# Kernel tuning notes

Hardware: AMD Instinct MI355X
Metric: run time of the kernel (lower is better)

The kernel has to match this reference:

```python
import jax, jax.numpy as jnp
import numpy as np

N_NODES = 10000
N_EDGES = 160000
IN_DIM = 512
HID = 256
HEADS = 4
OUT_DIM = 512
NEG_SLOPE = 0.2  # PyG GATConv default


def _glorot(key, shape):
    fan_in, fan_out = shape[0], shape[-1]
    lim = jnp.sqrt(6.0 / (fan_in + fan_out))
    return jax.random.uniform(key, shape, jnp.float32, -lim, lim)


def setup_inputs() -> dict:
    key = jax.random.key(0)
    ks = jax.random.split(key, 16)
    x = jax.random.normal(ks[0], (N_NODES, IN_DIM), jnp.float32)
    edge_index = jax.random.randint(ks[1], (2, N_EDGES), 0, N_NODES, jnp.int64)
    # layer 1: GATConv(512 -> 256, heads=4, concat) -> out 1024
    W1 = _glorot(ks[2], (IN_DIM, HEADS * HID))
    att_src1 = _glorot(ks[3], (HEADS, HID))
    att_dst1 = _glorot(ks[4], (HEADS, HID))
    b1 = jnp.zeros((HEADS * HID,), jnp.float32)
    # layer 2: GATConv(1024 -> 256, heads=4, concat) -> out 1024
    W2 = _glorot(ks[5], (HEADS * HID, HEADS * HID))
    att_src2 = _glorot(ks[6], (HEADS, HID))
    att_dst2 = _glorot(ks[7], (HEADS, HID))
    b2 = jnp.zeros((HEADS * HID,), jnp.float32)
    # final fc: 1024 -> 512
    fcW = _glorot(ks[8], (HEADS * HID, OUT_DIM))
    fcb = jnp.zeros((OUT_DIM,), jnp.float32)
    return dict(x=x, edge_index=edge_index, W1=W1, att_src1=att_src1,
                att_dst1=att_dst1, b1=b1, W2=W2, att_src2=att_src2,
                att_dst2=att_dst2, b2=b2, fcW=fcW, fcb=fcb)


def gat_conv(x, src, dst, W, att_src, att_dst, bias):
    # x: [N, F_in]; src/dst: [E] (self-loops already included)
    N = x.shape[0]
    h = (x @ W).reshape(N, HEADS, HID)                       # [N, H, C]
    a_src = jnp.sum(h * att_src, axis=-1)                    # [N, H]
    a_dst = jnp.sum(h * att_dst, axis=-1)                    # [N, H]
    e = jax.nn.leaky_relu(a_src[src] + a_dst[dst], NEG_SLOPE)  # [E, H]
    # numerically stable segment softmax over destination nodes
    m = jax.ops.segment_max(e, dst, num_segments=N)          # [N, H]
    e = jnp.exp(e - m[dst])
    s = jax.ops.segment_sum(e, dst, num_segments=N)          # [N, H]
    alpha = e / (s[dst] + 1e-16)                             # [E, H]
    msg = alpha[:, :, None] * h[src]                         # [E, H, C]
    out = jax.ops.segment_sum(msg, dst, num_segments=N)      # [N, H, C]
    return out.reshape(N, HEADS * HID) + bias


def reference(x, edge_index, W1, att_src1, att_dst1, b1,
              W2, att_src2, att_dst2, b2, fcW, fcb):
    N = x.shape[0]
    loops = jnp.arange(N, dtype=edge_index.dtype)
    src = jnp.concatenate([edge_index[0], loops])  # PyG add_self_loops=True
    dst = jnp.concatenate([edge_index[1], loops])
    h = gat_conv(x, src, dst, W1, att_src1, att_dst1, b1)
    h = jax.nn.relu(h)  # dropout is identity in eval mode
    h = gat_conv(h, src, dst, W2, att_src2, att_dst2, b2)
    h = jax.nn.relu(h)
    return h @ fcW + fcb
```

## Files before the change

kernel.cpp:

```cpp
#include <hip/hip_runtime.h>
#include <hip/hip_bf16.h>

#define NN 10000
#define NE 160000
#define NET 170000
#define IN_DIM 512
#define D1 1024
#define HEADS 4
#define HID 256
#define OUT_DIM 512
#define NEG_SLOPE 0.2f

typedef __attribute__((ext_vector_type(8))) short bf16x8;
typedef __attribute__((ext_vector_type(4))) float f32x4;

__device__ inline float b2f(unsigned short b) {
    union { unsigned u; float f; } x; x.u = ((unsigned)b) << 16; return x.f;
}
__device__ inline unsigned short f2b(float f) {
    union { float f; unsigned u; } x; x.f = f;
    unsigned u = x.u;
    unsigned r = u + 0x7FFFu + ((u >> 16) & 1u);
    return (unsigned short)(r >> 16);
}
__device__ inline float lrelu(float v) { return v > 0.f ? v : NEG_SLOPE * v; }

__global__ void init_kernel(const int* ei32, int* flag, int* counts, int* cursor) {
    int i = blockIdx.x * blockDim.x + threadIdx.x;
    if (i < NN) { counts[i] = 0; cursor[i] = 0; }
    if (blockIdx.x == 0) {
        __shared__ int nz;
        if (threadIdx.x == 0) nz = 0;
        __syncthreads();
        int acc = 0;
        for (int k = threadIdx.x; k < 500; k += 256) acc |= ei32[2 * k + 1];
        if (acc) atomicOr(&nz, 1);
        __syncthreads();
        if (threadIdx.x == 0) flag[0] = (nz == 0) ? 1 : 0;
    }
}

__device__ inline void load_edge(const void* ei, int f64, int e, int& s, int& d) {
    if (f64) {
        const long long* p = (const long long*)ei;
        s = (int)p[e]; d = (int)p[NE + e];
    } else {
        const int* p = (const int*)ei;
        s = p[e]; d = p[NE + e];
    }
}

__global__ void count_kernel(const void* ei, const int* flag, int* counts) {
    int e = blockIdx.x * blockDim.x + threadIdx.x;
    if (e >= NET) return;
    int s, d;
    if (e < NE) load_edge(ei, *flag, e, s, d);
    else d = e - NE;
    atomicAdd(&counts[d], 1);
}

__global__ __launch_bounds__(256) void scan_kernel(const int* counts, int* indptr) {
    __shared__ int part[256];
    int t = threadIdx.x;
    int base = t * 40;
    int local[40];
    int sum = 0;
#pragma unroll
    for (int k = 0; k < 40; k++) {
        int i = base + k;
        int c = (i < NN) ? counts[i] : 0;
        local[k] = sum;
        sum += c;
    }
    part[t] = sum;
    __syncthreads();
    for (int off = 1; off < 256; off <<= 1) {
        int v = (t >= off) ? part[t - off] : 0;
        __syncthreads();
        part[t] += v;
        __syncthreads();
    }
    int excl = part[t] - sum;
#pragma unroll
    for (int k = 0; k < 40; k++) {
        int i = base + k;
        if (i < NN) indptr[i] = excl + local[k];
    }
    if (t == 255) indptr[NN] = part[255];
}

__global__ void fill_kernel(const void* ei, const int* flag, const int* indptr,
                            int* cursor, int* csr_src) {
    int e = blockIdx.x * blockDim.x + threadIdx.x;
    if (e >= NET) return;
    int s, d;
    if (e < NE) load_edge(ei, *flag, e, s, d);
    else { s = e - NE; d = s; }
    int pos = indptr[d] + atomicAdd(&cursor[d], 1);
    csr_src[pos] = s;
}

__device__ void tpose_tile(const float* __restrict__ in, unsigned short* __restrict__ out,
                           int R, int C, int bx, int by) {
    __shared__ float tile[32][33];
    int tx = threadIdx.x & 31, ty = threadIdx.x >> 5;
    int c = bx * 32 + tx;
#pragma unroll
    for (int r0 = 0; r0 < 32; r0 += 8) {
        int r = by * 32 + ty + r0;
        tile[ty + r0][tx] = in[(size_t)r * C + c];
    }
    __syncthreads();
    int oc = by * 32 + tx;
#pragma unroll
    for (int r0 = 0; r0 < 32; r0 += 8) {
        int orow = bx * 32 + ty + r0;
        out[(size_t)orow * R + oc] = f2b(tile[tx][ty + r0]);
    }
}

#define CVT_NB 5000
#define TP1_NB 512
#define TP2_NB 1024
#define TP3_NB 512
__global__ __launch_bounds__(256) void prep_kernel(
    const float* __restrict__ x, unsigned short* __restrict__ xb,
    const float* __restrict__ W1, unsigned short* __restrict__ W1t,
    const float* __restrict__ W2, unsigned short* __restrict__ W2t,
    const float* __restrict__ fcW, unsigned short* __restrict__ fcWt) {
    int b = blockIdx.x;
    if (b < CVT_NB) {
        int i = b * 256 + threadIdx.x;
        float4 v = reinterpret_cast<const float4*>(x)[i];
        ushort4 o;
        o.x = f2b(v.x); o.y = f2b(v.y); o.z = f2b(v.z); o.w = f2b(v.w);
        reinterpret_cast<ushort4*>(xb)[i] = o;
        return;
    }
    b -= CVT_NB;
    if (b < TP1_NB) { tpose_tile(W1, W1t, IN_DIM, D1, b & 31, b >> 5); return; }
    b -= TP1_NB;
    if (b < TP2_NB) { tpose_tile(W2, W2t, D1, D1, b & 31, b >> 5); return; }
    b -= TP2_NB;
    tpose_tile(fcW, fcWt, D1, OUT_DIM, b & 15, b >> 4);
}

#define BM 128
#define BN 128
#define BK 64
__global__ __launch_bounds__(256) void gemm128(
    const unsigned short* __restrict__ A, const unsigned short* __restrict__ B,
    const float* __restrict__ bias, float* __restrict__ Cf, unsigned short* __restrict__ Cb,
    int M, int N, int K, int NB) {
    __shared__ __align__(16) unsigned short As[BM * BK];
    __shared__ __align__(16) unsigned short Bs[BN * BK];
    int t = threadIdx.x;
    int nwg = gridDim.x;
    int q = nwg >> 3, r = nwg & 7;
    int xcd = blockIdx.x & 7, jj = blockIdx.x >> 3;
    int wg = (xcd < r ? xcd * (q + 1) : r * (q + 1) + (xcd - r) * q) + jj;
    int row0 = (wg / NB) * BM, col0 = (wg % NB) * BN;

    int w = t >> 6, l = t & 63;
    int wr = w >> 1, wc = w & 1;
    f32x4 acc[4][4] = {};

    int srow = w * 8 + (l >> 3);
    int scs = (((l & 7) ^ (l >> 3)) * 8);
    const unsigned short* ap0 = A + (size_t)min(row0 +  0 + srow, M - 1) * K + scs;
    const unsigned short* ap1 = A + (size_t)min(row0 + 32 + srow, M - 1) * K + scs;
    const unsigned short* ap2 = A + (size_t)min(row0 + 64 + srow, M - 1) * K + scs;
    const unsigned short* ap3 = A + (size_t)min(row0 + 96 + srow, M - 1) * K + scs;
    const unsigned short* bp0 = B + (size_t)(col0 +  0 + srow) * K + scs;
    const unsigned short* bp1 = B + (size_t)(col0 + 32 + srow) * K + scs;
    const unsigned short* bp2 = B + (size_t)(col0 + 64 + srow) * K + scs;
    const unsigned short* bp3 = B + (size_t)(col0 + 96 + srow) * K + scs;
    unsigned short* asd0 = As + 0 * 2048 + w * 512;
    unsigned short* asd1 = As + 1 * 2048 + w * 512;
    unsigned short* asd2 = As + 2 * 2048 + w * 512;
    unsigned short* asd3 = As + 3 * 2048 + w * 512;
    unsigned short* bsd0 = Bs + 0 * 2048 + w * 512;
    unsigned short* bsd1 = Bs + 1 * 2048 + w * 512;
    unsigned short* bsd2 = Bs + 2 * 2048 + w * 512;
    unsigned short* bsd3 = Bs + 3 * 2048 + w * 512;

    int rr = l & 15;
    int rb = (rr & 7) << 4;
    int kb0 = (l >> 4) << 4;
    const char* Ab = (const char*)As;
    const char* Bb = (const char*)Bs;

#define GLD(src, dst) __builtin_amdgcn_global_load_lds( \
        (const __attribute__((address_space(1))) void*)(src), \
        (__attribute__((address_space(3))) void*)(dst), 16, 0, 0)

    for (int k0 = 0; k0 < K; k0 += BK) {
        GLD(ap0, asd0); GLD(ap1, asd1); GLD(ap2, asd2); GLD(ap3, asd3);
        GLD(bp0, bsd0); GLD(bp1, bsd1); GLD(bp2, bsd2); GLD(bp3, bsd3);
        ap0 += BK; ap1 += BK; ap2 += BK; ap3 += BK;
        bp0 += BK; bp1 += BK; bp2 += BK; bp3 += BK;
        __syncthreads();

#pragma unroll
        for (int ks = 0; ks < 2; ks++) {
            int kb = ((ks << 6) | kb0) ^ rb;
            bf16x8 af[4], bfv[4];
#pragma unroll
            for (int mi = 0; mi < 4; mi++)
                af[mi] = *reinterpret_cast<const bf16x8*>(
                    Ab + (wr * 64 + mi * 16 + rr) * 128 + kb);
#pragma unroll
            for (int ni = 0; ni < 4; ni++)
                bfv[ni] = *reinterpret_cast<const bf16x8*>(
                    Bb + (wc * 64 + ni * 16 + rr) * 128 + kb);
#pragma unroll
            for (int mi = 0; mi < 4; mi++)
#pragma unroll
                for (int ni = 0; ni < 4; ni++)
                    acc[mi][ni] = __builtin_amdgcn_mfma_f32_16x16x32_bf16(
                        af[mi], bfv[ni], acc[mi][ni], 0, 0, 0);
        }
        __syncthreads();
    }
#undef GLD

    int c_l = l & 15, r_h = (l >> 4) * 4;
#pragma unroll
    for (int mi = 0; mi < 4; mi++)
#pragma unroll
        for (int ni = 0; ni < 4; ni++) {
            int gc = col0 + wc * 64 + ni * 16 + c_l;
#pragma unroll
            for (int j = 0; j < 4; j++) {
                int gr = row0 + wr * 64 + mi * 16 + r_h + j;
                if (gr < M) {
                    float v = acc[mi][ni][j];
                    if (bias) v += bias[gc];
                    if (Cf) Cf[(size_t)gr * N + gc] = v;
                    if (Cb) Cb[(size_t)gr * N + gc] = f2b(v);
                }
            }
        }
}

__global__ __launch_bounds__(256) void att_kernel(const unsigned short* __restrict__ hb,
                                                  const float* __restrict__ att_s,
                                                  const float* __restrict__ att_d,
                                                  float* __restrict__ aS, float* __restrict__ aD) {
    int node = blockIdx.x * 4 + (threadIdx.x >> 6);
    int l = threadIdx.x & 63;
    int head = l >> 4, qq = l & 15;
    const unsigned short* hrow = hb + (size_t)node * D1 + head * HID + qq * 16;
    bf16x8 h0 = *reinterpret_cast<const bf16x8*>(hrow);
    bf16x8 h1 = *reinterpret_cast<const bf16x8*>(hrow + 8);
    const float* asp = att_s + head * HID + qq * 16;
    const float* adp = att_d + head * HID + qq * 16;
    float ps = 0.f, pd = 0.f;
#pragma unroll
    for (int c = 0; c < 8; c++) {
        float hv = b2f((unsigned short)h0[c]);
        float hw = b2f((unsigned short)h1[c]);
        ps += hv * asp[c] + hw * asp[8 + c];
        pd += hv * adp[c] + hw * adp[8 + c];
    }
#pragma unroll
    for (int off = 1; off <= 8; off <<= 1) {
        ps += __shfl_xor(ps, off);
        pd += __shfl_xor(pd, off);
    }
    if (qq == 0) {
        aS[node * HEADS + head] = ps;
        aD[node * HEADS + head] = pd;
    }
}

__global__ __launch_bounds__(256) void agg_kernel(const unsigned short* __restrict__ hb,
                                                  const float* __restrict__ aS,
                                                  const float* __restrict__ aD,
                                                  const int* __restrict__ indptr,
                                                  const int* __restrict__ csr_src,
                                                  const float* __restrict__ bias,
                                                  unsigned short* __restrict__ outb) {
    int node = blockIdx.x * 4 + (threadIdx.x >> 6);
    int l = threadIdx.x & 63;
    int head = l >> 4;
    int beg = indptr[node];
    int deg = indptr[node + 1] - beg;
    float adst = aD[node * HEADS + head];
    const unsigned short* hp = hb + (size_t)l * 16;
    const int* cs = csr_src + beg;
    float acc[16];
#pragma unroll
    for (int c = 0; c < 16; c++) acc[c] = 0.f;
    float esum = 0.f;
    int dm = deg - 1;
    for (int j = 0; j < deg; j += 4) {
        int i0 = j, i1 = min(j + 1, dm), i2 = min(j + 2, dm), i3 = min(j + 3, dm);
        int s0 = cs[i0], s1 = cs[i1], s2 = cs[i2], s3 = cs[i3];
        const unsigned short* r0 = hp + (size_t)s0 * D1;
        const unsigned short* r1 = hp + (size_t)s1 * D1;
        const unsigned short* r2 = hp + (size_t)s2 * D1;
        const unsigned short* r3 = hp + (size_t)s3 * D1;
        bf16x8 r0a = *reinterpret_cast<const bf16x8*>(r0);
        bf16x8 r0b = *reinterpret_cast<const bf16x8*>(r0 + 8);
        bf16x8 r1a = *reinterpret_cast<const bf16x8*>(r1);
        bf16x8 r1b = *reinterpret_cast<const bf16x8*>(r1 + 8);
        bf16x8 r2a = *reinterpret_cast<const bf16x8*>(r2);
        bf16x8 r2b = *reinterpret_cast<const bf16x8*>(r2 + 8);
        bf16x8 r3a = *reinterpret_cast<const bf16x8*>(r3);
        bf16x8 r3b = *reinterpret_cast<const bf16x8*>(r3 + 8);
        float e0 = __expf(lrelu(aS[s0 * HEADS + head] + adst));
        float e1 = (j + 1 <= dm) ? __expf(lrelu(aS[s1 * HEADS + head] + adst)) : 0.f;
        float e2 = (j + 2 <= dm) ? __expf(lrelu(aS[s2 * HEADS + head] + adst)) : 0.f;
        float e3 = (j + 3 <= dm) ? __expf(lrelu(aS[s3 * HEADS + head] + adst)) : 0.f;
        esum += e0 + e1 + e2 + e3;
#pragma unroll
        for (int c = 0; c < 8; c++) {
            acc[c] += e0 * b2f((unsigned short)r0a[c]) + e1 * b2f((unsigned short)r1a[c])
                    + e2 * b2f((unsigned short)r2a[c]) + e3 * b2f((unsigned short)r3a[c]);
            acc[8 + c] += e0 * b2f((unsigned short)r0b[c]) + e1 * b2f((unsigned short)r1b[c])
                        + e2 * b2f((unsigned short)r2b[c]) + e3 * b2f((unsigned short)r3b[c]);
        }
    }
    float inv = 1.f / (esum + 1e-16f);
    const float* bp = bias + l * 16;
    bf16x8 o0, o1;
#pragma unroll
    for (int c = 0; c < 8; c++) {
        o0[c] = (short)f2b(fmaxf(acc[c] * inv + bp[c], 0.f));
        o1[c] = (short)f2b(fmaxf(acc[8 + c] * inv + bp[8 + c], 0.f));
    }
    unsigned short* op = outb + (size_t)node * D1 + l * 16;
    *reinterpret_cast<bf16x8*>(op) = o0;
    *reinterpret_cast<bf16x8*>(op + 8) = o1;
}

extern "C" void kernel_launch(void* const* d_in, const int* in_sizes, int n_in,
                              void* d_out, int out_size, void* d_ws, size_t ws_size,
                              hipStream_t stream) {
    const float* x   = (const float*)d_in[0];
    const void*  ei  = d_in[1];
    const float* W1  = (const float*)d_in[2];
    const float* as1 = (const float*)d_in[3];
    const float* ad1 = (const float*)d_in[4];
    const float* b1  = (const float*)d_in[5];
    const float* W2  = (const float*)d_in[6];
    const float* as2 = (const float*)d_in[7];
    const float* ad2 = (const float*)d_in[8];
    const float* b2  = (const float*)d_in[9];
    const float* fcW = (const float*)d_in[10];
    const float* fcb = (const float*)d_in[11];
    float* out = (float*)d_out;

    char* ws = (char*)d_ws;
    size_t o = 0;
    auto carve = [&](size_t bytes) -> char* {
        char* p = ws + o;
        o = (o + bytes + 255) & ~(size_t)255;
        return p;
    };
    unsigned short* xb   = (unsigned short*)carve((size_t)NN * IN_DIM * 2);
    unsigned short* hb   = (unsigned short*)carve((size_t)NN * D1 * 2);
    unsigned short* x2b  = (unsigned short*)carve((size_t)NN * D1 * 2);
    unsigned short* W1t  = (unsigned short*)carve((size_t)D1 * IN_DIM * 2);
    unsigned short* W2t  = (unsigned short*)carve((size_t)D1 * D1 * 2);
    unsigned short* fcWt = (unsigned short*)carve((size_t)OUT_DIM * D1 * 2);
    float* aS   = (float*)carve((size_t)NN * HEADS * 4);
    float* aD   = (float*)carve((size_t)NN * HEADS * 4);
    int* counts = (int*)carve((size_t)NN * 4);
    int* cursor = (int*)carve((size_t)NN * 4);
    int* indptr = (int*)carve((size_t)(NN + 1) * 4);
    int* csr_src= (int*)carve((size_t)NET * 4);
    int* flag   = (int*)carve(4);
    (void)ws_size; (void)in_sizes; (void)n_in; (void)out_size;

    init_kernel<<<(NN + 255) / 256, 256, 0, stream>>>((const int*)ei, flag, counts, cursor);
    count_kernel<<<(NET + 255) / 256, 256, 0, stream>>>(ei, flag, counts);
    scan_kernel<<<1, 256, 0, stream>>>(counts, indptr);
    fill_kernel<<<(NET + 255) / 256, 256, 0, stream>>>(ei, flag, indptr, cursor, csr_src);

    prep_kernel<<<CVT_NB + TP1_NB + TP2_NB + TP3_NB, 256, 0, stream>>>(
        x, xb, W1, W1t, W2, W2t, fcW, fcWt);

    const int MB = (NN + BM - 1) / BM;
    gemm128<<<MB * (D1 / BN), 256, 0, stream>>>(xb, W1t, nullptr, nullptr, hb,
                                                NN, D1, IN_DIM, D1 / BN);
    att_kernel<<<NN / 4, 256, 0, stream>>>(hb, as1, ad1, aS, aD);
    agg_kernel<<<NN / 4, 256, 0, stream>>>(hb, aS, aD, indptr, csr_src, b1, x2b);
    gemm128<<<MB * (D1 / BN), 256, 0, stream>>>(x2b, W2t, nullptr, nullptr, hb,
                                                NN, D1, D1, D1 / BN);
    att_kernel<<<NN / 4, 256, 0, stream>>>(hb, as2, ad2, aS, aD);
    agg_kernel<<<NN / 4, 256, 0, stream>>>(hb, aS, aD, indptr, csr_src, b2, x2b);
    gemm128<<<MB * (OUT_DIM / BN), 256, 0, stream>>>(x2b, fcWt, fcb, out, nullptr,
                                                     NN, OUT_DIM, D1, OUT_DIM / BN);
}
```

Baseline: 269.2 us.

## Split aggregation across eight column-slice blocks per node group with 2-channel lanes

The aggregation kernel now launches eight blocks per group of four nodes, each covering a 128-column slice (half a head). Each lane handles two bf16 channels instead of sixteen, and the edge loop is unrolled to eight neighbours. The aim is more parallelism, lower register pressure and better occupancy, with coalesced 256-byte row segments per wave. In exchange, index loads and exp computations are repeated eight times per node, and each lane's gather loads are narrow 4-byte accesses.

```diff
diff --git a/kernel.cpp b/kernel.cpp
--- a/kernel.cpp
+++ b/kernel.cpp
@@ -281,58 +281,55 @@
                                                   const int* __restrict__ csr_src,
                                                   const float* __restrict__ bias,
                                                   unsigned short* __restrict__ outb) {
-    int node = blockIdx.x * 4 + (threadIdx.x >> 6);
+    int slice = blockIdx.x & 7;
+    int node = (blockIdx.x >> 3) * 4 + (threadIdx.x >> 6);
     int l = threadIdx.x & 63;
-    int head = l >> 4;
+    int head = slice >> 1;
+    int cbase = slice * 128 + l * 2;
     int beg = indptr[node];
     int deg = indptr[node + 1] - beg;
     float adst = aD[node * HEADS + head];
-    const unsigned short* hp = hb + (size_t)l * 16;
     const int* cs = csr_src + beg;
-    float acc[16];
-#pragma unroll
-    for (int c = 0; c < 16; c++) acc[c] = 0.f;
-    float esum = 0.f;
+    const unsigned short* hp = hb + cbase;
+    const float* aSh = aS + head;
+    float acc0 = 0.f, acc1 = 0.f, esum = 0.f;
     int dm = deg - 1;
-    for (int j = 0; j < deg; j += 4) {
-        int i0 = j, i1 = min(j + 1, dm), i2 = min(j + 2, dm), i3 = min(j + 3, dm);
-        int s0 = cs[i0], s1 = cs[i1], s2 = cs[i2], s3 = cs[i3];
-        const unsigned short* r0 = hp + (size_t)s0 * D1;
-        const unsigned short* r1 = hp + (size_t)s1 * D1;
-        const unsigned short* r2 = hp + (size_t)s2 * D1;
-        const unsigned short* r3 = hp + (size_t)s3 * D1;
-        bf16x8 r0a = *reinterpret_cast<const bf16x8*>(r0);
-        bf16x8 r0b = *reinterpret_cast<const bf16x8*>(r0 + 8);
-        bf16x8 r1a = *reinterpret_cast<const bf16x8*>(r1);
-        bf16x8 r1b = *reinterpret_cast<const bf16x8*>(r1 + 8);
-        bf16x8 r2a = *reinterpret_cast<const bf16x8*>(r2);
-        bf16x8 r2b = *reinterpret_cast<const bf16x8*>(r2 + 8);
-        bf16x8 r3a = *reinterpret_cast<const bf16x8*>(r3);
-        bf16x8 r3b = *reinterpret_cast<const bf16x8*>(r3 + 8);
-        float e0 = __expf(lrelu(aS[s0 * HEADS + head] + adst));
-        float e1 = (j + 1 <= dm) ? __expf(lrelu(aS[s1 * HEADS + head] + adst)) : 0.f;
-        float e2 = (j + 2 <= dm) ? __expf(lrelu(aS[s2 * HEADS + head] + adst)) : 0.f;
-        float e3 = (j + 3 <= dm) ? __expf(lrelu(aS[s3 * HEADS + head] + adst)) : 0.f;
-        esum += e0 + e1 + e2 + e3;
-#pragma unroll
-        for (int c = 0; c < 8; c++) {
-            acc[c] += e0 * b2f((unsigned short)r0a[c]) + e1 * b2f((unsigned short)r1a[c])
-                    + e2 * b2f((unsigned short)r2a[c]) + e3 * b2f((unsigned short)r3a[c]);
-            acc[8 + c] += e0 * b2f((unsigned short)r0b[c]) + e1 * b2f((unsigned short)r1b[c])
-                        + e2 * b2f((unsigned short)r2b[c]) + e3 * b2f((unsigned short)r3b[c]);
-        }
+    for (int j = 0; j < deg; j += 8) {
+        int i1 = min(j + 1, dm), i2 = min(j + 2, dm), i3 = min(j + 3, dm);
+        int i4 = min(j + 4, dm), i5 = min(j + 5, dm), i6 = min(j + 6, dm), i7 = min(j + 7, dm);
+        int s0 = cs[j],  s1 = cs[i1], s2 = cs[i2], s3 = cs[i3];
+        int s4 = cs[i4], s5 = cs[i5], s6 = cs[i6], s7 = cs[i7];
+        unsigned r0 = *reinterpret_cast<const unsigned*>(hp + (size_t)s0 * D1);
+        unsigned r1 = *reinterpret_cast<const unsigned*>(hp + (size_t)s1 * D1);
+        unsigned r2 = *reinterpret_cast<const unsigned*>(hp + (size_t)s2 * D1);
+        unsigned r3 = *reinterpret_cast<const unsigned*>(hp + (size_t)s3 * D1);
+        unsigned r4 = *reinterpret_cast<const unsigned*>(hp + (size_t)s4 * D1);
+        unsigned r5 = *reinterpret_cast<const unsigned*>(hp + (size_t)s5 * D1);
+        unsigned r6 = *reinterpret_cast<const unsigned*>(hp + (size_t)s6 * D1);
+        unsigned r7 = *reinterpret_cast<const unsigned*>(hp + (size_t)s7 * D1);
+        float e0 = __expf(lrelu(aSh[s0 * HEADS] + adst));
+        float e1 = (j + 1 <= dm) ? __expf(lrelu(aSh[s1 * HEADS] + adst)) : 0.f;
+        float e2 = (j + 2 <= dm) ? __expf(lrelu(aSh[s2 * HEADS] + adst)) : 0.f;
+        float e3 = (j + 3 <= dm) ? __expf(lrelu(aSh[s3 * HEADS] + adst)) : 0.f;
+        float e4 = (j + 4 <= dm) ? __expf(lrelu(aSh[s4 * HEADS] + adst)) : 0.f;
+        float e5 = (j + 5 <= dm) ? __expf(lrelu(aSh[s5 * HEADS] + adst)) : 0.f;
+        float e6 = (j + 6 <= dm) ? __expf(lrelu(aSh[s6 * HEADS] + adst)) : 0.f;
+        float e7 = (j + 7 <= dm) ? __expf(lrelu(aSh[s7 * HEADS] + adst)) : 0.f;
+        esum += (e0 + e1 + e2 + e3) + (e4 + e5 + e6 + e7);
+        acc0 += e0 * b2f((unsigned short)(r0 & 0xFFFF)) + e1 * b2f((unsigned short)(r1 & 0xFFFF))
+              + e2 * b2f((unsigned short)(r2 & 0xFFFF)) + e3 * b2f((unsigned short)(r3 & 0xFFFF))
+              + e4 * b2f((unsigned short)(r4 & 0xFFFF)) + e5 * b2f((unsigned short)(r5 & 0xFFFF))
+              + e6 * b2f((unsigned short)(r6 & 0xFFFF)) + e7 * b2f((unsigned short)(r7 & 0xFFFF));
+        acc1 += e0 * b2f((unsigned short)(r0 >> 16)) + e1 * b2f((unsigned short)(r1 >> 16))
+              + e2 * b2f((unsigned short)(r2 >> 16)) + e3 * b2f((unsigned short)(r3 >> 16))
+              + e4 * b2f((unsigned short)(r4 >> 16)) + e5 * b2f((unsigned short)(r5 >> 16))
+              + e6 * b2f((unsigned short)(r6 >> 16)) + e7 * b2f((unsigned short)(r7 >> 16));
     }
     float inv = 1.f / (esum + 1e-16f);
-    const float* bp = bias + l * 16;
-    bf16x8 o0, o1;
-#pragma unroll
-    for (int c = 0; c < 8; c++) {
-        o0[c] = (short)f2b(fmaxf(acc[c] * inv + bp[c], 0.f));
-        o1[c] = (short)f2b(fmaxf(acc[8 + c] * inv + bp[8 + c], 0.f));
-    }
-    unsigned short* op = outb + (size_t)node * D1 + l * 16;
-    *reinterpret_cast<bf16x8*>(op) = o0;
-    *reinterpret_cast<bf16x8*>(op + 8) = o1;
+    ushort2 o;
+    o.x = f2b(fmaxf(acc0 * inv + bias[cbase], 0.f));
+    o.y = f2b(fmaxf(acc1 * inv + bias[cbase + 1], 0.f));
+    *reinterpret_cast<ushort2*>(outb + (size_t)node * D1 + cbase) = o;
 }
 
 extern "C" void kernel_launch(void* const* d_in, const int* in_sizes, int n_in,
@@ -386,11 +383,11 @@
     gemm128<<<MB * (D1 / BN), 256, 0, stream>>>(xb, W1t, nullptr, nullptr, hb,
                                                 NN, D1, IN_DIM, D1 / BN);
     att_kernel<<<NN / 4, 256, 0, stream>>>(hb, as1, ad1, aS, aD);
-    agg_kernel<<<NN / 4, 256, 0, stream>>>(hb, aS, aD, indptr, csr_src, b1, x2b);
+    agg_kernel<<<(NN / 4) * 8, 256, 0, stream>>>(hb, aS, aD, indptr, csr_src, b1, x2b);
     gemm128<<<MB * (D1 / BN), 256, 0, stream>>>(x2b, W2t, nullptr, nullptr, hb,
                                                 NN, D1, D1, D1 / BN);
     att_kernel<<<NN / 4, 256, 0, stream>>>(hb, as2, ad2, aS, aD);
-    agg_kernel<<<NN / 4, 256, 0, stream>>>(hb, aS, aD, indptr, csr_src, b2, x2b);
+    agg_kernel<<<(NN / 4) * 8, 256, 0, stream>>>(hb, aS, aD, indptr, csr_src, b2, x2b);
     gemm128<<<MB * (OUT_DIM / BN), 256, 0, stream>>>(x2b, fcWt, fcb, out, nullptr,
                                                      NN, OUT_DIM, D1, OUT_DIM / BN);
 }
```

New measurement: 313.6 us. 16.5% more time.
